# Optimization experiments

Hardware: AMD Instinct MI355X
Metric: run time of the kernel (lower is better)

Reference implementation:

```python
import jax, jax.numpy as jnp
import numpy as np

B, N, FIN, FOUT, E = 2, 50000, 128, 64, 800000


def setup_inputs() -> dict:
    key = jax.random.key(0)
    ks = jax.random.split(key, 7)
    x = jax.random.normal(ks[0], (B, N, FIN), dtype=jnp.float32)
    W = jax.random.normal(ks[1], (FIN, FOUT), dtype=jnp.float32) * (1.0 / np.sqrt(FIN))
    W_self = jax.random.normal(ks[2], (FIN, FOUT), dtype=jnp.float32) * (1.0 / np.sqrt(FIN))
    b_self = jax.random.normal(ks[3], (FOUT,), dtype=jnp.float32) * 0.01
    edge_row = jax.random.randint(ks[4], (E,), 0, N, dtype=jnp.int32)
    edge_col = jax.random.randint(ks[5], (E,), 0, N, dtype=jnp.int32)
    edge_val = jax.random.uniform(ks[6], (E,), dtype=jnp.float32)
    return {"x": x, "W": W, "W_self": W_self, "b_self": b_self,
            "edge_row": edge_row, "edge_col": edge_col, "edge_val": edge_val}


def reference(x, W, W_self, b_self, edge_row, edge_col, edge_val):
    # x: (B, N, FIN); adjacency in COO form: out[r] += val * in[c]
    Bn, Nn, _ = x.shape
    Fo = W.shape[1]
    x_trans = jnp.einsum("bnf,fo->bno", x, W)               # (B, N, FOUT), no bias
    # Same layout trick as torch: sparse.mm over (N, B*FOUT)
    xr = x_trans.transpose(1, 0, 2).reshape(Nn, Bn * Fo)    # (N, B*FOUT)
    msgs = edge_val[:, None] * xr[edge_col]                  # (E, B*FOUT) gather
    agg = jax.ops.segment_sum(msgs, edge_row, num_segments=Nn)  # (N, B*FOUT) scatter-add
    agg = agg.reshape(Nn, Bn, Fo).transpose(1, 0, 2)         # (B, N, FOUT)
    self_c = jnp.einsum("bnf,fo->bno", x, W_self) + b_self   # Linear with bias
    return jax.nn.relu(self_c + agg)
```

## Files before the change

### kernel.cpp

```cpp
#include <hip/hip_runtime.h>
#include <hip/hip_fp16.h>

#define Bc   2
#define Nn   50000
#define FINc 128
#define FOUTc 64
#define Mtot (Bc * Nn)
#define CCOMB 128
#define GB 1563
#define SB 1563
#define CAP 64
#define ZTOT (Nn * 16)

typedef __bf16 bf16x8 __attribute__((ext_vector_type(8)));
typedef float  f32x4  __attribute__((ext_vector_type(4)));

static __device__ inline unsigned short f2bf(float f) {
    unsigned int u = __float_as_uint(f);
    u += 0x7fffu + ((u >> 16) & 1u);
    return (unsigned short)(u >> 16);
}

__global__ __launch_bounds__(256) void prep(
    const float* __restrict__ W, const float* __restrict__ Ws,
    unsigned short* __restrict__ Bp, int* __restrict__ zbase)
{
    if (blockIdx.x < 8) {
        const int idx = blockIdx.x * 256 + threadIdx.x;
        const int lane = idx & 63;
        const int kt   = (idx >> 6) & 3;
        const int nt   = idx >> 8;
        const int n    = nt * 16 + (lane & 15);
        const int k0   = kt * 32 + (lane >> 4) * 8;
        unsigned short o8[8];
#pragma unroll
        for (int j = 0; j < 8; ++j) {
            const int f = k0 + j;
            const float v = (n < 64) ? W[f * FOUTc + n] : Ws[f * FOUTc + (n - 64)];
            o8[j] = f2bf(v);
        }
        *(uint4*)&Bp[(size_t)idx * 8] = *(uint4*)o8;
    } else {
        const int i4 = (blockIdx.x - 8) * 1024 + threadIdx.x * 4;
        if (i4 + 4 <= ZTOT)
            *(int4*)&zbase[i4] = make_int4(0, 0, 0, 0);
    }
}

__global__ __launch_bounds__(256) void scatter_gemm(
    const float* __restrict__ x, const unsigned short* __restrict__ Bp,
    const float* __restrict__ bself,
    unsigned short* __restrict__ xrb, float* __restrict__ outp,
    const int* __restrict__ erow, const int* __restrict__ ecol,
    const float* __restrict__ evalv, int* __restrict__ cntp,
    unsigned int* __restrict__ cvp, int E)
{
    const int b = blockIdx.x;

    if (!(b & 1)) {
        const int sb = b >> 1;
        const int e0 = sb * 512 + threadIdx.x;
        const int e1 = e0 + 256;
        if (e0 < E) {
            const int   r = erow[e0];
            const int   c = ecol[e0];
            const float v = evalv[e0];
            const int k = atomicAdd(&cntp[(size_t)r * 16], 1);
            if (k < CAP)
                cvp[((size_t)r << 6) + k] =
                    ((unsigned int)__half_as_ushort(__float2half(v)) << 17) | (unsigned int)c;
        }
        if (e1 < E) {
            const int   r = erow[e1];
            const int   c = ecol[e1];
            const float v = evalv[e1];
            const int k = atomicAdd(&cntp[(size_t)r * 16], 1);
            if (k < CAP)
                cvp[((size_t)r << 6) + k] =
                    ((unsigned int)__half_as_ushort(__float2half(v)) << 17) | (unsigned int)c;
        }
        return;
    }

    const int gb   = b >> 1;
    const int lane = threadIdx.x & 63;
    const int quad = lane >> 4;
    const int mbase = gb * 64 + (threadIdx.x >> 6) * 16;

    const int mrow   = mbase + (lane & 15);
    const int mclamp = (mrow < Mtot) ? mrow : (Mtot - 1);
    const float* __restrict__ xrow = &x[(size_t)mclamp * FINc + quad * 8];

    float4 xv[8];
#pragma unroll
    for (int kt = 0; kt < 4; ++kt) {
        xv[2 * kt]     = *(const float4*)&xrow[kt * 32];
        xv[2 * kt + 1] = *(const float4*)&xrow[kt * 32 + 4];
    }

    f32x4 acc[8] = {};

#pragma unroll
    for (int kt = 0; kt < 4; ++kt) {
        const float4 xa = xv[2 * kt];
        const float4 xb = xv[2 * kt + 1];
        bf16x8 bf;
        bf[0] = (__bf16)xa.x; bf[1] = (__bf16)xa.y;
        bf[2] = (__bf16)xa.z; bf[3] = (__bf16)xa.w;
        bf[4] = (__bf16)xb.x; bf[5] = (__bf16)xb.y;
        bf[6] = (__bf16)xb.z; bf[7] = (__bf16)xb.w;

        const bf16x8* __restrict__ abase =
            (const bf16x8*)&Bp[(size_t)(kt * 64 + lane) * 8];
#pragma unroll
        for (int nt = 0; nt < 8; ++nt) {
            const bf16x8 af = abase[nt * 4 * 64];
            acc[nt] = __builtin_amdgcn_mfma_f32_16x16x32_bf16(af, bf, acc[nt], 0, 0, 0);
        }
    }

    const int m = mbase + (lane & 15);
    if (m < Mtot) {
        const int bb = (m >= Nn) ? 1 : 0;
        const int n = m - bb * Nn;
        unsigned short* __restrict__ xp = &xrb[(size_t)n * CCOMB + bb * FOUTc];
        const int cq = quad * 4;
#pragma unroll
        for (int nt = 0; nt < 4; ++nt) {
            const int c = nt * 16 + cq;
            unsigned short h[4];
            h[0] = f2bf(acc[nt][0]); h[1] = f2bf(acc[nt][1]);
            h[2] = f2bf(acc[nt][2]); h[3] = f2bf(acc[nt][3]);
            *(uint2*)&xp[c] = *(uint2*)h;
        }
        float* __restrict__ op = &outp[(size_t)m * FOUTc];
#pragma unroll
        for (int nt = 4; nt < 8; ++nt) {
            const int o = (nt - 4) * 16 + cq;
            const float4 b4 = *(const float4*)&bself[o];
            float4 v;
            v.x = acc[nt][0] + b4.x; v.y = acc[nt][1] + b4.y;
            v.z = acc[nt][2] + b4.z; v.w = acc[nt][3] + b4.w;
            *(float4*)&op[o] = v;
        }
    }
}

#define GATHP(W, PRED, ACC)                                                   \
    {                                                                         \
        const unsigned int w = (W);                                           \
        unsigned int col = w & 0x1FFFFu;                                      \
        col = (col < Nn) ? col : 0u;           \
        const float vv = (PRED) ? __half2float(__ushort_as_half(              \
                             (unsigned short)(w >> 17))) : 0.0f;              \
        const uint4 raw = *(const uint4*)&xrb[(size_t)col * CCOMB + c0];      \
        ACC[0] = fmaf(vv, __uint_as_float(raw.x << 16),         ACC[0]);      \
        ACC[1] = fmaf(vv, __uint_as_float(raw.x & 0xffff0000u), ACC[1]);      \
        ACC[2] = fmaf(vv, __uint_as_float(raw.y << 16),         ACC[2]);      \
        ACC[3] = fmaf(vv, __uint_as_float(raw.y & 0xffff0000u), ACC[3]);      \
        ACC[4] = fmaf(vv, __uint_as_float(raw.z << 16),         ACC[4]);      \
        ACC[5] = fmaf(vv, __uint_as_float(raw.z & 0xffff0000u), ACC[5]);      \
        ACC[6] = fmaf(vv, __uint_as_float(raw.w << 16),         ACC[6]);      \
        ACC[7] = fmaf(vv, __uint_as_float(raw.w & 0xffff0000u), ACC[7]);      \
    }

__global__ __launch_bounds__(256) void row_gather(
    const int* __restrict__ cntp, const unsigned int* __restrict__ cvp,
    const unsigned short* __restrict__ xrb, float* __restrict__ outp)
{
    const int j    = blockIdx.x;
    const int low3 = j & 7;
    const int h    = (low3 >= 4) ? 1 : 0;
    const int ord  = (j >> 3) * 4 + (low3 & 3);
    int n = ord * 4 + (threadIdx.x >> 6);
    n = __builtin_amdgcn_readfirstlane(n);

    const int lane = threadIdx.x & 63;
    const int slot = lane >> 3;
    const int c0   = h * 64 + (lane & 7) * 8;
    const unsigned int* __restrict__ seg = &cvp[(size_t)n << 6];

    const int kc = min(cntp[(size_t)n * 16], CAP);
    const unsigned int u0 = seg[slot];
    const unsigned int u1 = seg[8 + slot];

    float aA[8] = {0.f, 0.f, 0.f, 0.f, 0.f, 0.f, 0.f, 0.f};

    GATHP(u0, slot < kc,     aA);
    GATHP(u1, slot + 8 < kc, aA);

    for (int e = 16 + slot; e < kc; e += 8) {
        const unsigned int u = seg[e];
        GATHP(u, true, aA);
    }

#pragma unroll
    for (int i = 0; i < 8; ++i) {
        aA[i] += __shfl_down(aA[i], 8);
        aA[i] += __shfl_down(aA[i], 16);
        aA[i] += __shfl_down(aA[i], 32);
    }

    if (lane < 8) {
        const size_t m = (size_t)h * Nn + n;
        const int o = lane * 8;
        float* __restrict__ op = &outp[m * FOUTc + o];
        float4 s0 = *(float4*)&op[0];
        float4 s1 = *(float4*)&op[4];
        s0.x = fmaxf(s0.x + aA[0], 0.0f); s0.y = fmaxf(s0.y + aA[1], 0.0f);
        s0.z = fmaxf(s0.z + aA[2], 0.0f); s0.w = fmaxf(s0.w + aA[3], 0.0f);
        s1.x = fmaxf(s1.x + aA[4], 0.0f); s1.y = fmaxf(s1.y + aA[5], 0.0f);
        s1.z = fmaxf(s1.z + aA[6], 0.0f); s1.w = fmaxf(s1.w + aA[7], 0.0f);
        *(float4*)&op[0] = s0;
        *(float4*)&op[4] = s1;
    }
}

extern "C" void kernel_launch(void* const* d_in, const int* in_sizes, int n_in,
                              void* d_out, int out_size, void* d_ws, size_t ws_size,
                              hipStream_t stream)
{
    const float* x    = (const float*)d_in[0];
    const float* W    = (const float*)d_in[1];
    const float* Ws   = (const float*)d_in[2];
    const float* bs   = (const float*)d_in[3];
    const int*   erow = (const int*)d_in[4];
    const int*   ecol = (const int*)d_in[5];
    const float* eval = (const float*)d_in[6];
    float* outp = (float*)d_out;
    const int E = in_sizes[4];

    unsigned short* xrb = (unsigned short*)d_ws;
    unsigned int*   cvp = (unsigned int*)(xrb + (size_t)Nn * CCOMB);
    int*            cntp = (int*)(cvp + ((size_t)Nn << 6));
    unsigned short* Bp  = (unsigned short*)(cntp + (size_t)Nn * 16);

    prep<<<8 + (ZTOT + 1023) / 1024, 256, 0, stream>>>(W, Ws, Bp, cntp);

    scatter_gemm<<<SB + GB, 256, 0, stream>>>(x, Bp, bs, xrb, outp,
                                              erow, ecol, eval, cntp, cvp, E);

    row_gather<<<Nn / 2, 256, 0, stream>>>(cntp, cvp, xrb, outp);
}
```

Baseline: 194.5 us.

## Fuse three kernels into one cooperative persistent kernel with grid syncs

Merges the prep, scatter/GEMM and row-gather kernels into a single persistent cooperative kernel of 1024 blocks. Each phase loops over its original block indices and the phases are separated by grid-wide barriers. The aim is to remove two kernel launch boundaries and their tail effects. In exchange it pays grid.sync costs, host-side occupancy and attribute queries on every call, and fewer resident blocks than the original grids. If the cooperative launch is unavailable it falls back to the three separate kernels.

```diff
diff --git a/kernel.cpp b/kernel.cpp
--- a/kernel.cpp
+++ b/kernel.cpp
@@ -1,5 +1,8 @@
 #include <hip/hip_runtime.h>
 #include <hip/hip_fp16.h>
+#include <hip/hip_cooperative_groups.h>
+
+namespace cg = cooperative_groups;
 
 #define Bc   2
 #define Nn   50000
@@ -11,6 +14,8 @@
 #define SB 1563
 #define CAP 64
 #define ZTOT (Nn * 16)
+#define GRID 1024
+#define PREPB (8 + (ZTOT + 1023) / 1024)
 
 typedef __bf16 bf16x8 __attribute__((ext_vector_type(8)));
 typedef float  f32x4  __attribute__((ext_vector_type(4)));
@@ -21,12 +26,13 @@
     return (unsigned short)(u >> 16);
 }
 
-__global__ __launch_bounds__(256) void prep(
-    const float* __restrict__ W, const float* __restrict__ Ws,
-    unsigned short* __restrict__ Bp, int* __restrict__ zbase)
-{
-    if (blockIdx.x < 8) {
-        const int idx = blockIdx.x * 256 + threadIdx.x;
+
+static __device__ inline void prep_body(int i, const float* __restrict__ W,
+    const float* __restrict__ Ws, unsigned short* __restrict__ Bp,
+    int* __restrict__ cntp)
+{
+    if (i < 8) {
+        const int idx = i * 256 + threadIdx.x;
         const int lane = idx & 63;
         const int kt   = (idx >> 6) & 3;
         const int nt   = idx >> 8;
@@ -41,13 +47,13 @@
         }
         *(uint4*)&Bp[(size_t)idx * 8] = *(uint4*)o8;
     } else {
-        const int i4 = (blockIdx.x - 8) * 1024 + threadIdx.x * 4;
+        const int i4 = (i - 8) * 1024 + threadIdx.x * 4;
         if (i4 + 4 <= ZTOT)
-            *(int4*)&zbase[i4] = make_int4(0, 0, 0, 0);
-    }
-}
-
-__global__ __launch_bounds__(256) void scatter_gemm(
+            *(int4*)&cntp[i4] = make_int4(0, 0, 0, 0);
+    }
+}
+
+static __device__ inline void scatter_gemm_body(int i,
     const float* __restrict__ x, const unsigned short* __restrict__ Bp,
     const float* __restrict__ bself,
     unsigned short* __restrict__ xrb, float* __restrict__ outp,
@@ -55,10 +61,8 @@
     const float* __restrict__ evalv, int* __restrict__ cntp,
     unsigned int* __restrict__ cvp, int E)
 {
-    const int b = blockIdx.x;
-
-    if (!(b & 1)) {
-        const int sb = b >> 1;
+    if (!(i & 1)) {
+        const int sb = i >> 1;
         const int e0 = sb * 512 + threadIdx.x;
         const int e1 = e0 + 256;
         if (e0 < E) {
@@ -82,7 +86,7 @@
         return;
     }
 
-    const int gb   = b >> 1;
+    const int gb   = i >> 1;
     const int lane = threadIdx.x & 63;
     const int quad = lane >> 4;
     const int mbase = gb * 64 + (threadIdx.x >> 6) * 16;
@@ -164,11 +168,10 @@
         ACC[7] = fmaf(vv, __uint_as_float(raw.w & 0xffff0000u), ACC[7]);      \
     }
 
-__global__ __launch_bounds__(256) void row_gather(
+static __device__ inline void row_gather_body(int j,
     const int* __restrict__ cntp, const unsigned int* __restrict__ cvp,
     const unsigned short* __restrict__ xrb, float* __restrict__ outp)
 {
-    const int j    = blockIdx.x;
     const int low3 = j & 7;
     const int h    = (low3 >= 4) ? 1 : 0;
     const int ord  = (j >> 3) * 4 + (low3 & 3);
@@ -216,6 +219,59 @@
     }
 }
 
+__global__ __launch_bounds__(256, 4) void fused_all(
+    const float* __restrict__ x, const float* __restrict__ W,
+    const float* __restrict__ Ws, const float* __restrict__ bself,
+    const int* __restrict__ erow, const int* __restrict__ ecol,
+    const float* __restrict__ evalv,
+    unsigned short* __restrict__ xrb, float* __restrict__ outp,
+    int* __restrict__ cntp, unsigned int* __restrict__ cvp,
+    unsigned short* __restrict__ Bp, int E)
+{
+    cg::grid_group grid = cg::this_grid();
+    const int b = blockIdx.x;
+
+    for (int i = b; i < PREPB; i += GRID)
+        prep_body(i, W, Ws, Bp, cntp);
+    __threadfence();
+    grid.sync();
+
+    for (int i = b; i < SB + GB; i += GRID)
+        scatter_gemm_body(i, x, Bp, bself, xrb, outp, erow, ecol, evalv,
+                          cntp, cvp, E);
+    __threadfence();
+    grid.sync();
+
+    for (int j = b; j < Nn / 2; j += GRID)
+        row_gather_body(j, cntp, cvp, xrb, outp);
+}
+
+__global__ __launch_bounds__(256) void prep_k(
+    const float* __restrict__ W, const float* __restrict__ Ws,
+    unsigned short* __restrict__ Bp, int* __restrict__ cntp)
+{
+    prep_body(blockIdx.x, W, Ws, Bp, cntp);
+}
+
+__global__ __launch_bounds__(256) void scatter_gemm_k(
+    const float* __restrict__ x, const unsigned short* __restrict__ Bp,
+    const float* __restrict__ bself,
+    unsigned short* __restrict__ xrb, float* __restrict__ outp,
+    const int* __restrict__ erow, const int* __restrict__ ecol,
+    const float* __restrict__ evalv, int* __restrict__ cntp,
+    unsigned int* __restrict__ cvp, int E)
+{
+    scatter_gemm_body(blockIdx.x, x, Bp, bself, xrb, outp, erow, ecol, evalv,
+                      cntp, cvp, E);
+}
+
+__global__ __launch_bounds__(256) void row_gather_k(
+    const int* __restrict__ cntp, const unsigned int* __restrict__ cvp,
+    const unsigned short* __restrict__ xrb, float* __restrict__ outp)
+{
+    row_gather_body(blockIdx.x, cntp, cvp, xrb, outp);
+}
+
 extern "C" void kernel_launch(void* const* d_in, const int* in_sizes, int n_in,
                               void* d_out, int out_size, void* d_ws, size_t ws_size,
                               hipStream_t stream)
@@ -228,17 +284,39 @@
     const int*   ecol = (const int*)d_in[5];
     const float* eval = (const float*)d_in[6];
     float* outp = (float*)d_out;
-    const int E = in_sizes[4];
+    int E = in_sizes[4];
 
     unsigned short* xrb = (unsigned short*)d_ws;
     unsigned int*   cvp = (unsigned int*)(xrb + (size_t)Nn * CCOMB);
     int*            cntp = (int*)(cvp + ((size_t)Nn << 6));
     unsigned short* Bp  = (unsigned short*)(cntp + (size_t)Nn * 16);
 
-    prep<<<8 + (ZTOT + 1023) / 1024, 256, 0, stream>>>(W, Ws, Bp, cntp);
-
-    scatter_gemm<<<SB + GB, 256, 0, stream>>>(x, Bp, bs, xrb, outp,
-                                              erow, ecol, eval, cntp, cvp, E);
-
-    row_gather<<<Nn / 2, 256, 0, stream>>>(cntp, cvp, xrb, outp);
-}
+    int dev = 0;
+    hipGetDevice(&dev);
+    int coop = 0;
+    hipDeviceGetAttribute(&coop, hipDeviceAttributeCooperativeLaunch, dev);
+    int maxBlk = 0;
+    hipError_t occ_rc = hipOccupancyMaxActiveBlocksPerMultiprocessor(
+        &maxBlk, (const void*)fused_all, 256, 0);
+
+    bool used_coop = false;
+    if (coop && occ_rc == hipSuccess && (long long)maxBlk * 256 >= GRID) {
+        void* args[] = {
+            (void*)&x, (void*)&W, (void*)&Ws, (void*)&bs,
+            (void*)&erow, (void*)&ecol, (void*)&eval,
+            (void*)&xrb, (void*)&outp, (void*)&cntp, (void*)&cvp,
+            (void*)&Bp, (void*)&E
+        };
+        hipError_t rc = hipLaunchCooperativeKernel((const void*)fused_all,
+                                                   dim3(GRID), dim3(256),
+                                                   args, 0, stream);
+        used_coop = (rc == hipSuccess);
+    }
+
+    if (!used_coop) {
+        prep_k<<<PREPB, 256, 0, stream>>>(W, Ws, Bp, cntp);
+        scatter_gemm_k<<<SB + GB, 256, 0, stream>>>(x, Bp, bs, xrb, outp,
+                                                    erow, ecol, eval, cntp, cvp, E);
+        row_gather_k<<<Nn / 2, 256, 0, stream>>>(cntp, cvp, xrb, outp);
+    }
+}
```

Result: no change. 195.7 us (+0.6%).
